# Optimization experiments

Measured on AMD Instinct MI355X. Metric: run time of the kernel, lower is better.

## Reference

```python
import jax, jax.numpy as jnp
import numpy as np

B, S = 64, 1024
DC, DR, H, DA = 64, 64, 128, 128
NC, NQ, MC = 256, 10000, 4


def setup_inputs() -> dict:
    key = jax.random.key(0)
    ks = jax.random.split(key, 16)
    question_seq = jax.random.randint(ks[0], (B, S), 0, NQ)
    correctness_seq = jax.random.randint(ks[1], (B, S), 0, 2)
    q2c_table = jax.random.randint(ks[2], (NQ, MC), 0, NC)
    q2c_mask = jax.random.randint(ks[3], (NQ, MC), 0, 2).at[:, 0].set(1)  # >=1 concept per question
    sd = 0.02
    concept_embed = jax.random.normal(ks[4], (NC, DC), jnp.float32) * sd
    correctness_embed = jax.random.normal(ks[5], (2, DR), jnp.float32) * sd
    mlp_w = jax.random.normal(ks[6], (DA, H), jnp.float32) * (1.0 / np.sqrt(H))
    mlp_b = jnp.zeros((DA,), jnp.float32)
    sim_w = jax.random.normal(ks[7], (1, DA), jnp.float32) * (1.0 / np.sqrt(DA))
    DIN = DC + DR
    W_ih = jax.random.normal(ks[8], (3 * H, DIN), jnp.float32) * (1.0 / np.sqrt(H))
    b_ih = jnp.zeros((3 * H,), jnp.float32)
    W_hh = jax.random.normal(ks[9], (3 * H, H), jnp.float32) * (1.0 / np.sqrt(H))
    b_hh = jnp.zeros((3 * H,), jnp.float32)
    pred_w = jax.random.normal(ks[10], (1, 2 * H + DC), jnp.float32) * (1.0 / np.sqrt(2 * H + DC))
    pred_b = jnp.zeros((1,), jnp.float32)
    return dict(question_seq=question_seq, correctness_seq=correctness_seq,
                q2c_table=q2c_table, q2c_mask=q2c_mask,
                concept_embed=concept_embed, correctness_embed=correctness_embed,
                mlp_w=mlp_w, mlp_b=mlp_b, sim_w=sim_w,
                W_ih=W_ih, b_ih=b_ih, W_hh=W_hh, b_hh=b_hh,
                pred_w=pred_w, pred_b=pred_b)


def _concept_emb(question_seq, q2c_table, q2c_mask, concept_embed):
    # fused question->concept embedding: masked mean over mapped concepts
    cids = q2c_table[question_seq]                      # [B,S,MC]
    m = q2c_mask[question_seq].astype(jnp.float32)      # [B,S,MC]
    ce = concept_embed[cids]                            # [B,S,MC,DC]
    return (ce * m[..., None]).sum(2) / jnp.clip(m.sum(2), 1.0)[..., None]


def _gru(x, W_ih, b_ih, W_hh, b_hh):
    # torch nn.GRU equations, batch_first; x: [B,S,DIN] -> [B,S,H]
    Xp = jnp.einsum('bsd,gd->bsg', x, W_ih) + b_ih      # [B,S,3H]
    h0 = jnp.zeros((x.shape[0], H), x.dtype)

    def step(h, gi):
        gh = h @ W_hh.T + b_hh
        i_r, i_z, i_n = jnp.split(gi, 3, axis=-1)
        h_r, h_z, h_n = jnp.split(gh, 3, axis=-1)
        r = jax.nn.sigmoid(i_r + h_r)
        z = jax.nn.sigmoid(i_z + h_z)
        n = jnp.tanh(i_n + r * h_n)
        h_new = (1.0 - z) * n + z * h
        return h_new, h_new

    _, hs = jax.lax.scan(step, h0, Xp.transpose(1, 0, 2))
    return hs.transpose(1, 0, 2)


def _attention(rnn_out, mlp_w, mlp_b, sim_w):
    # additive per-key score, causal softmax, bmm, exclusive cumsum, concat
    s = jnp.einsum('bsa,oa->bso', jnp.tanh(jnp.einsum('bsh,ah->bsa', rnn_out, mlp_w) + mlp_b), sim_w)[..., 0]  # [B,S]
    seq = rnn_out.shape[1]
    causal = jnp.tril(jnp.ones((seq, seq), bool))       # keep j<=i
    scores = jnp.where(causal[None], s[:, None, :], -jnp.inf)  # [B,S,S]
    alphas = jax.nn.softmax(scores, axis=-1)
    attn = jnp.einsum('bij,bjh->bih', alphas, rnn_out)  # [B,S,H]
    excl = jnp.cumsum(attn, axis=1) - attn              # exclusive cumsum
    return jnp.concatenate([excl, rnn_out], axis=-1)    # [B,S,2H]


def reference(question_seq, correctness_seq, q2c_table, q2c_mask,
              concept_embed, correctness_embed, mlp_w, mlp_b, sim_w,
              W_ih, b_ih, W_hh, b_hh, pred_w, pred_b):
    concept = _concept_emb(question_seq, q2c_table, q2c_mask, concept_embed)  # [B,S,DC]
    corr = correctness_embed[correctness_seq]                                  # [B,S,DR]
    cc = jnp.concatenate([concept, corr], -1)
    rc = jnp.concatenate([corr, concept], -1)
    inter = jnp.where((correctness_seq == 1)[..., None], cc, rc)               # [B,S,DC+DR]
    rnn_out = _gru(inter, W_ih, b_ih, W_hh, b_hh)                              # [B,S,H]
    latent = _attention(rnn_out, mlp_w, mlp_b, sim_w)                          # [B,S,2H]
    pin = jnp.concatenate([latent[:, :-1], concept[:, 1:]], axis=-1)           # [B,S-1,2H+DC]
    logits = jnp.einsum('bsd,od->bso', pin, pred_w) + pred_b
    return jax.nn.sigmoid(logits)[..., 0]                                      # [B,S-1]
```

## Files before the change

### kernel.cpp

```cpp
#include <hip/hip_runtime.h>
#include <hip/hip_bf16.h>
#include <cstdint>

#define BB 64
#define SS 1024
#define DCn 64
#define Hn 128
#define G3 384
#define HPITCH 144

using f32x4 = __attribute__((ext_vector_type(4))) float;
using bf16x8 = __attribute__((ext_vector_type(8))) short;

__device__ __forceinline__ float sigmoid_f(float x) {
  return __builtin_amdgcn_rcpf(1.0f + __expf(-x));
}
__device__ __forceinline__ float tanh_f(float x) {
  float xc = fminf(fmaxf(x, -15.0f), 15.0f);
  float t = __expf(-2.0f * xc);
  return (1.0f - t) * __builtin_amdgcn_rcpf(1.0f + t);
}
__device__ __forceinline__ short f2bf(float x) {
  union { float f; uint32_t u; } v; v.f = x;
  uint32_t r = v.u + 0x7FFFu + ((v.u >> 16) & 1u);
  return (short)(r >> 16);
}
__device__ __forceinline__ float bf2f(ushort u) {
  union { uint32_t i; float f; } v; v.i = (uint32_t)u << 16; return v.f;
}
__device__ __forceinline__ float sel4(f32x4 v, int q) {
  float t0 = (q & 1) ? v[1] : v[0];
  float t1 = (q & 1) ? v[3] : v[2];
  return (q & 2) ? t1 : t0;
}

#define LDS_BARRIER() do {                                   \
    asm volatile("s_waitcnt lgkmcnt(0)" ::: "memory");       \
    __builtin_amdgcn_s_barrier();                            \
    __builtin_amdgcn_sched_barrier(0);                       \
  } while (0)

__global__ __launch_bounds__(256) void convw_kernel(
    const float* __restrict__ W_ih, const float* __restrict__ mlp_w,
    const float* __restrict__ pred_w,
    ushort* __restrict__ Wihb, ushort* __restrict__ Baug) {
  int i = blockIdx.x * 256 + threadIdx.x;
  if (i < 49152) { Wihb[i] = (ushort)f2bf(W_ih[i]); return; }
  int j = i - 49152;
  int r = j >> 7, k = j & 127;
  float v = (r < 128) ? mlp_w[j]
          : (r == 128) ? pred_w[k]
          : (r == 129) ? pred_w[128 + k] : 0.0f;
  Baug[j] = (ushort)f2bf(v);
}

__global__ __launch_bounds__(256) void embed_kernel(
    const int* __restrict__ qseq, const int* __restrict__ cseq,
    const int* __restrict__ q2c, const int* __restrict__ q2cm,
    const float* __restrict__ cemb, const float* __restrict__ remb,
    const float* __restrict__ pred_w,
    ushort* __restrict__ interb, float* __restrict__ C3) {
  int pos = blockIdx.x * 2 + (threadIdx.x >> 7);
  int d = threadIdx.x & 127;
  int q = qseq[pos];
  int corr = cseq[pos];
  float val;
  if (d < 64) {
    float acc = 0.f, msum = 0.f;
#pragma unroll
    for (int c = 0; c < 4; ++c) {
      int id = q2c[q * 4 + c];
      float m = (float)q2cm[q * 4 + c];
      acc += m * cemb[id * 64 + d];
      msum += m;
    }
    val = acc / fmaxf(msum, 1.0f);
    float p3 = val * pred_w[256 + d];
#pragma unroll
    for (int o = 32; o; o >>= 1) p3 += __shfl_down(p3, o);
    if (d == 0) C3[pos] = p3;
  } else {
    val = remb[corr * 64 + (d - 64)];
  }
  int slot = (corr == 1) ? d : ((d < 64) ? d + 64 : d - 64);
  interb[(size_t)pos * 128 + slot] = (ushort)f2bf(val);
}

__global__ __launch_bounds__(256) void gemm_mfma_kernel(
    const ushort* __restrict__ Ap, const ushort* __restrict__ Bp,
    const float* __restrict__ bias, ushort* __restrict__ Cp, int N) {
  __shared__ bf16x8 Al[64][16];
  __shared__ bf16x8 Bl[64][16];
  const int m0 = blockIdx.x * 64, n0 = blockIdx.y * 64;
  const int tid = threadIdx.x;
  const int row = tid >> 2, j0 = (tid & 3) * 4;
  {
    const bf16x8* A = (const bf16x8*)Ap + (size_t)(m0 + row) * 16 + j0;
#pragma unroll
    for (int jj = 0; jj < 4; ++jj) Al[row][(j0 + jj) ^ (row & 15)] = A[jj];
    const bf16x8* Bg = (const bf16x8*)Bp + (size_t)(n0 + row) * 16 + j0;
#pragma unroll
    for (int jj = 0; jj < 4; ++jj) Bl[row][(j0 + jj) ^ (row & 15)] = Bg[jj];
  }
  __syncthreads();
  const int w = tid >> 6, lane = tid & 63, ln = lane & 15, cc = lane >> 4;
  bf16x8 bfr[4];
#pragma unroll
  for (int ks = 0; ks < 4; ++ks) bfr[ks] = Bl[w * 16 + ln][(ks * 4 + cc) ^ ln];
  f32x4 C0 = {0,0,0,0}, C1 = {0,0,0,0}, C2 = {0,0,0,0}, C3v = {0,0,0,0};
#pragma unroll
  for (int ks = 0; ks < 4; ++ks) {
    bf16x8 a0 = Al[0 * 16 + ln][(ks * 4 + cc) ^ ln];
    bf16x8 a1 = Al[1 * 16 + ln][(ks * 4 + cc) ^ ln];
    bf16x8 a2 = Al[2 * 16 + ln][(ks * 4 + cc) ^ ln];
    bf16x8 a3 = Al[3 * 16 + ln][(ks * 4 + cc) ^ ln];
    C0 = __builtin_amdgcn_mfma_f32_16x16x32_bf16(a0, bfr[ks], C0, 0, 0, 0);
    C1 = __builtin_amdgcn_mfma_f32_16x16x32_bf16(a1, bfr[ks], C1, 0, 0, 0);
    C2 = __builtin_amdgcn_mfma_f32_16x16x32_bf16(a2, bfr[ks], C2, 0, 0, 0);
    C3v = __builtin_amdgcn_mfma_f32_16x16x32_bf16(a3, bfr[ks], C3v, 0, 0, 0);
  }
  const float bv = bias[n0 + w * 16 + ln];
  const size_t ncol = n0 + w * 16 + ln;
#pragma unroll
  for (int rt = 0; rt < 4; ++rt) {
    f32x4 Cf = (rt == 0) ? C0 : (rt == 1) ? C1 : (rt == 2) ? C2 : C3v;
#pragma unroll
    for (int q = 0; q < 4; ++q)
      Cp[(size_t)(m0 + rt * 16 + cc * 4 + q) * N + ncol] = (ushort)f2bf(Cf[q] + bv);
  }
}

__global__ __attribute__((amdgpu_flat_work_group_size(512, 512)))
__attribute__((amdgpu_waves_per_eu(2, 2))) void gru_kernel(
    const ushort* __restrict__ Xp, const float* __restrict__ W_hh,
    const float* __restrict__ b_hh, float* __restrict__ rnn_out) {
  const int tid = threadIdx.x;
  const int w = tid >> 6;
  const int lane = tid & 63;
  const int ln = lane & 15;
  const int c = lane >> 4;
  const int bl = ln & 3;
  const int qs = ln >> 2;
  const int b0 = blockIdx.x * 4;

  __shared__ alignas(16) short hlds[2][4 * HPITCH];

  bf16x8 wf[3][4];
#pragma unroll
  for (int gt = 0; gt < 3; ++gt) {
    const float* wr = W_hh + (size_t)(gt * 128 + w * 16 + ln) * 128 + c * 8;
#pragma unroll
    for (int ks = 0; ks < 4; ++ks) {
      bf16x8 f;
#pragma unroll
      for (int j = 0; j < 8; ++j) f[j] = f2bf(wr[ks * 32 + j]);
      wf[gt][ks] = f;
    }
  }
  const f32x4 br = *(const f32x4*)(b_hh + w * 16 + c * 4);
  const f32x4 bz = *(const f32x4*)(b_hh + 128 + w * 16 + c * 4);
  const f32x4 bn = *(const f32x4*)(b_hh + 256 + w * 16 + c * 4);

  for (int i = tid; i < 576; i += 512) ((uint32_t*)hlds)[i] = 0;

  const int dim = w * 16 + c * 4 + qs;
  const ushort* xs = Xp + (size_t)(b0 + bl) * SS * G3 + dim;
  float* rsp = rnn_out + (size_t)(b0 + bl) * SS * Hn + dim;

  ushort xr0 = xs[0], xz0 = xs[128], xn0 = xs[256];
  ushort xr1 = xs[G3 + 0], xz1 = xs[G3 + 128], xn1 = xs[G3 + 256];
  const ushort* xpf = xs + 2 * (size_t)G3;

  float h_old = 0.0f;
  LDS_BARRIER();

#define GRU_STEP(RB, XR, XZ, XN)                                             \
  {                                                                          \
    const short* hr = hlds[RB] + bl * HPITCH;                                \
    bf16x8 h0 = *(const bf16x8*)(hr + 0 * 32 + c * 8);                       \
    bf16x8 h1 = *(const bf16x8*)(hr + 1 * 32 + c * 8);                       \
    bf16x8 h2 = *(const bf16x8*)(hr + 2 * 32 + c * 8);                       \
    bf16x8 h3 = *(const bf16x8*)(hr + 3 * 32 + c * 8);                       \
    ushort pr = xpf[0], pz = xpf[128], pn = xpf[256];                        \
    xpf += G3;                                                               \
    __builtin_amdgcn_s_setprio(1);                                           \
    f32x4 ar = br, az = bz, an = bn;                                         \
    ar = __builtin_amdgcn_mfma_f32_16x16x32_bf16(wf[0][0], h0, ar, 0, 0, 0); \
    an = __builtin_amdgcn_mfma_f32_16x16x32_bf16(wf[2][0], h0, an, 0, 0, 0); \
    ar = __builtin_amdgcn_mfma_f32_16x16x32_bf16(wf[0][1], h1, ar, 0, 0, 0); \
    an = __builtin_amdgcn_mfma_f32_16x16x32_bf16(wf[2][1], h1, an, 0, 0, 0); \
    ar = __builtin_amdgcn_mfma_f32_16x16x32_bf16(wf[0][2], h2, ar, 0, 0, 0); \
    an = __builtin_amdgcn_mfma_f32_16x16x32_bf16(wf[2][2], h2, an, 0, 0, 0); \
    ar = __builtin_amdgcn_mfma_f32_16x16x32_bf16(wf[0][3], h3, ar, 0, 0, 0); \
    an = __builtin_amdgcn_mfma_f32_16x16x32_bf16(wf[2][3], h3, an, 0, 0, 0); \
    az = __builtin_amdgcn_mfma_f32_16x16x32_bf16(wf[1][0], h0, az, 0, 0, 0); \
    az = __builtin_amdgcn_mfma_f32_16x16x32_bf16(wf[1][1], h1, az, 0, 0, 0); \
    az = __builtin_amdgcn_mfma_f32_16x16x32_bf16(wf[1][2], h2, az, 0, 0, 0); \
    az = __builtin_amdgcn_mfma_f32_16x16x32_bf16(wf[1][3], h3, az, 0, 0, 0); \
    __builtin_amdgcn_s_setprio(0);                                           \
    float ga = sel4(ar, qs), gz = sel4(az, qs), gn = sel4(an, qs);           \
    float r = sigmoid_f(bf2f(XR) + ga);                                      \
    float a = bf2f(XN) + r * gn;                                             \
    float e = __expf(-2.0f * a);                                             \
    float n = 2.0f * __builtin_amdgcn_rcpf(1.0f + e) - 1.0f;                 \
    float z = sigmoid_f(bf2f(XZ) + gz);                                      \
    float hn = n + z * (h_old - n);                                          \
    h_old = hn;                                                              \
    hlds[RB ^ 1][bl * HPITCH + dim] = f2bf(hn);                              \
    LDS_BARRIER();                                                           \
    *rsp = hn;                                                               \
    rsp += Hn;                                                               \
    XR = pr; XZ = pz; XN = pn;                                               \
  }

  for (int t = 0; t < SS; t += 2) {
    GRU_STEP(0, xr0, xz0, xn0)
    GRU_STEP(1, xr1, xz1, xn1)
  }
#undef GRU_STEP
}

__global__ __launch_bounds__(256) void gemm_score_kernel(
    const float* __restrict__ rnn, const ushort* __restrict__ Baug,
    const float* __restrict__ mlp_b, const float* __restrict__ sim_w,
    float* __restrict__ s, float* __restrict__ D1, float* __restrict__ D2) {
  __shared__ bf16x8 Al[64][16];
  __shared__ bf16x8 Bl[144][16];
  __shared__ float srow[64][4];
  const int m0 = blockIdx.x * 64;
  const int tid = threadIdx.x;
  {
    const int row = tid >> 2, j0 = (tid & 3) * 4;
    const float* A = rnn + (size_t)(m0 + row) * 128 + j0 * 8;
#pragma unroll
    for (int jj = 0; jj < 4; ++jj) {
      f32x4 lo = *(const f32x4*)(A + jj * 8);
      f32x4 hi = *(const f32x4*)(A + jj * 8 + 4);
      bf16x8 v;
#pragma unroll
      for (int q = 0; q < 4; ++q) { v[q] = f2bf(lo[q]); v[4 + q] = f2bf(hi[q]); }
      Al[row][(j0 + jj) ^ (row & 15)] = v;
    }
  }
  {
    const bf16x8* Bg = (const bf16x8*)Baug;
    for (int i = tid; i < 144 * 16; i += 256) {
      int r = i >> 4, j = i & 15;
      Bl[r][j ^ (r & 15)] = Bg[i];
    }
  }
  __syncthreads();
  const int w = tid >> 6, lane = tid & 63, ln = lane & 15, cc = lane >> 4;
  float racc[4][4] = {};
  for (int nt = w; nt < 9; nt += 4) {
    bf16x8 bfr[4];
#pragma unroll
    for (int ks = 0; ks < 4; ++ks) bfr[ks] = Bl[nt * 16 + ln][(ks * 4 + cc) ^ ln];
    f32x4 C0 = {0,0,0,0}, C1 = {0,0,0,0}, C2 = {0,0,0,0}, C3v = {0,0,0,0};
#pragma unroll
    for (int ks = 0; ks < 4; ++ks) {
      bf16x8 a0 = Al[0 * 16 + ln][(ks * 4 + cc) ^ ln];
      bf16x8 a1 = Al[1 * 16 + ln][(ks * 4 + cc) ^ ln];
      bf16x8 a2 = Al[2 * 16 + ln][(ks * 4 + cc) ^ ln];
      bf16x8 a3 = Al[3 * 16 + ln][(ks * 4 + cc) ^ ln];
      C0 = __builtin_amdgcn_mfma_f32_16x16x32_bf16(a0, bfr[ks], C0, 0, 0, 0);
      C1 = __builtin_amdgcn_mfma_f32_16x16x32_bf16(a1, bfr[ks], C1, 0, 0, 0);
      C2 = __builtin_amdgcn_mfma_f32_16x16x32_bf16(a2, bfr[ks], C2, 0, 0, 0);
      C3v = __builtin_amdgcn_mfma_f32_16x16x32_bf16(a3, bfr[ks], C3v, 0, 0, 0);
    }
    if (nt < 8) {
      const int col = nt * 16 + ln;
      const float bv = mlp_b[col];
      const float sw = sim_w[col];
#pragma unroll
      for (int rt = 0; rt < 4; ++rt) {
        f32x4 Cf = (rt == 0) ? C0 : (rt == 1) ? C1 : (rt == 2) ? C2 : C3v;
#pragma unroll
        for (int q = 0; q < 4; ++q)
          racc[rt][q] += tanh_f(Cf[q] + bv) * sw;
      }
    } else if (ln < 2) {
      float* Dp = (ln == 0) ? D1 : D2;
#pragma unroll
      for (int rt = 0; rt < 4; ++rt) {
        f32x4 Cf = (rt == 0) ? C0 : (rt == 1) ? C1 : (rt == 2) ? C2 : C3v;
#pragma unroll
        for (int q = 0; q < 4; ++q)
          Dp[m0 + rt * 16 + cc * 4 + q] = Cf[q];
      }
    }
  }
#pragma unroll
  for (int o = 1; o <= 8; o <<= 1)
#pragma unroll
    for (int rt = 0; rt < 4; ++rt)
#pragma unroll
      for (int q = 0; q < 4; ++q)
        racc[rt][q] += __shfl_xor(racc[rt][q], o);
  if (ln == 0)
#pragma unroll
    for (int rt = 0; rt < 4; ++rt)
#pragma unroll
      for (int q = 0; q < 4; ++q)
        srow[rt * 16 + cc * 4 + q][w] = racc[rt][q];
  __syncthreads();
  if (tid < 64)
    s[m0 + tid] = srow[tid][0] + srow[tid][1] + srow[tid][2] + srow[tid][3];
}

__global__ __launch_bounds__(128) void attn_final_kernel(
    const float* __restrict__ s, const float* __restrict__ D1,
    const float* __restrict__ D2, const float* __restrict__ C3,
    const float* __restrict__ pred_b, float* __restrict__ out) {
  const int b = blockIdx.x;
  const int tid = threadIdx.x;
  __shared__ float elds[SS];
  __shared__ float rcpd[SS];
  __shared__ float d1l[SS];
  __shared__ float dcl[SS];
  __shared__ float red[2];
  __shared__ float wtot[2];
  const float pb = pred_b[0];
  const float* sb = s + (size_t)b * SS;
  const float* d1b = D1 + (size_t)b * SS;
  const float* d2b = D2 + (size_t)b * SS;
  const float* c3b = C3 + (size_t)b * SS;
  float m = -1e30f;
  for (int i = tid; i < SS; i += 128) m = fmaxf(m, sb[i]);
#pragma unroll
  for (int o = 32; o; o >>= 1) m = fmaxf(m, __shfl_xor(m, o));
  if ((tid & 63) == 0) red[tid >> 6] = m;
  __syncthreads();
  m = fmaxf(red[0], red[1]);
  for (int i = tid; i < SS; i += 128) {
    elds[i] = __expf(sb[i] - m);
    d1l[i] = d1b[i];
    dcl[i] = d2b[i] + ((i < SS - 1) ? c3b[i + 1] : 0.0f) + pb;
  }
  __syncthreads();
  {
    const int base = tid * 8;
    float v[8];
    float run = 0.f;
#pragma unroll
    for (int k = 0; k < 8; ++k) { run += elds[base + k]; v[k] = run; }
    float tot = run, sc = tot;
#pragma unroll
    for (int o = 1; o < 64; o <<= 1) {
      float u = __shfl_up(sc, o);
      if ((tid & 63) >= o) sc += u;
    }
    if ((tid & 63) == 63) wtot[tid >> 6] = sc;
    __syncthreads();
    float excl = sc - tot;
    if (tid >= 64) excl += wtot[0];
#pragma unroll
    for (int k = 0; k < 8; ++k)
      rcpd[base + k] = __builtin_amdgcn_rcpf(v[k] + excl);
  }
  __syncthreads();
  float P_num = 0.f, P_run = 0.f;
  float* ob = out + (size_t)b * (SS - 1);
  for (int t = 0; t < SS; t += 4) {
    f32x4 e4 = *(const f32x4*)&elds[t];
    f32x4 r4 = *(const f32x4*)&rcpd[t];
    f32x4 d4 = *(const f32x4*)&d1l[t];
    f32x4 c4 = *(const f32x4*)&dcl[t];
#pragma unroll
    for (int k = 0; k < 4; ++k) {
      P_num += e4[k] * d4[k];
      float v = sigmoid_f(P_run + c4[k]);
      if (tid == 0 && (t + k) < SS - 1) ob[t + k] = v;
      P_run += P_num * r4[k];
    }
  }
}

extern "C" void kernel_launch(void* const* d_in, const int* in_sizes, int n_in,
                              void* d_out, int out_size, void* d_ws, size_t ws_size,
                              hipStream_t stream) {
  const int* qseq = (const int*)d_in[0];
  const int* cseq = (const int*)d_in[1];
  const int* q2c = (const int*)d_in[2];
  const int* q2cm = (const int*)d_in[3];
  const float* cemb = (const float*)d_in[4];
  const float* remb = (const float*)d_in[5];
  const float* mlp_w = (const float*)d_in[6];
  const float* mlp_b = (const float*)d_in[7];
  const float* sim_w = (const float*)d_in[8];
  const float* W_ih = (const float*)d_in[9];
  const float* b_ih = (const float*)d_in[10];
  const float* W_hh = (const float*)d_in[11];
  const float* b_hh = (const float*)d_in[12];
  const float* pred_w = (const float*)d_in[13];
  const float* pred_b = (const float*)d_in[14];
  float* out = (float*)d_out;

  float* ws = (float*)d_ws;
  ushort* interb = (ushort*)ws;
  ushort* Xp = (ushort*)(ws + 4194304);
  float* rnn = ws + 16777216;
  ushort* Wihb = (ushort*)(ws + 25165824);
  ushort* Baug = (ushort*)(ws + 25190400);
  float* sbuf = ws + 25199616;
  float* D1 = ws + 25265152;
  float* D2 = ws + 25330688;
  float* C3 = ws + 25396224;

  convw_kernel<<<264, 256, 0, stream>>>(W_ih, mlp_w, pred_w, Wihb, Baug);
  embed_kernel<<<32768, 256, 0, stream>>>(qseq, cseq, q2c, q2cm, cemb, remb,
                                          pred_w, interb, C3);
  gemm_mfma_kernel<<<dim3(1024, 6), 256, 0, stream>>>(interb, Wihb, b_ih, Xp, 384);
  gru_kernel<<<16, 512, 0, stream>>>(Xp, W_hh, b_hh, rnn);
  gemm_score_kernel<<<1024, 256, 0, stream>>>(rnn, Baug, mlp_b, sim_w,
                                              sbuf, D1, D2);
  attn_final_kernel<<<64, 128, 0, stream>>>(sbuf, D1, D2, C3, pred_b, out);
}
```

Baseline: 509.4 us.

## Fuse embedding into input-projection GEMM and store GRU output as bf16

Embedding gather and the W_ih projection GEMM now run in one kernel: each 512-thread block builds its 64-row bf16 input tile directly in LDS and multiplies it against the full 384-column W_ih held in LDS. This removes the interb round trip through global memory and one kernel launch. Separately, the GRU writes its hidden-state output as bf16 instead of fp32, so the score GEMM loads bf16 directly and skips its conversion step. The costs are a larger LDS footprint per block and a serialized embedding phase before the MFMA work.

```diff
diff --git a/kernel.cpp b/kernel.cpp
--- a/kernel.cpp
+++ b/kernel.cpp
@@ -54,86 +54,87 @@
   Baug[j] = (ushort)f2bf(v);
 }
 
-__global__ __launch_bounds__(256) void embed_kernel(
+__global__ __attribute__((amdgpu_flat_work_group_size(512, 512))) void embgemm_kernel(
     const int* __restrict__ qseq, const int* __restrict__ cseq,
     const int* __restrict__ q2c, const int* __restrict__ q2cm,
     const float* __restrict__ cemb, const float* __restrict__ remb,
-    const float* __restrict__ pred_w,
-    ushort* __restrict__ interb, float* __restrict__ C3) {
-  int pos = blockIdx.x * 2 + (threadIdx.x >> 7);
-  int d = threadIdx.x & 127;
-  int q = qseq[pos];
-  int corr = cseq[pos];
-  float val;
-  if (d < 64) {
-    float acc = 0.f, msum = 0.f;
-#pragma unroll
-    for (int c = 0; c < 4; ++c) {
-      int id = q2c[q * 4 + c];
-      float m = (float)q2cm[q * 4 + c];
-      acc += m * cemb[id * 64 + d];
-      msum += m;
-    }
-    val = acc / fmaxf(msum, 1.0f);
-    float p3 = val * pred_w[256 + d];
-#pragma unroll
-    for (int o = 32; o; o >>= 1) p3 += __shfl_down(p3, o);
-    if (d == 0) C3[pos] = p3;
-  } else {
-    val = remb[corr * 64 + (d - 64)];
-  }
-  int slot = (corr == 1) ? d : ((d < 64) ? d + 64 : d - 64);
-  interb[(size_t)pos * 128 + slot] = (ushort)f2bf(val);
-}
-
-__global__ __launch_bounds__(256) void gemm_mfma_kernel(
-    const ushort* __restrict__ Ap, const ushort* __restrict__ Bp,
-    const float* __restrict__ bias, ushort* __restrict__ Cp, int N) {
+    const float* __restrict__ pred_w, const ushort* __restrict__ Wihb,
+    const float* __restrict__ b_ih,
+    ushort* __restrict__ Xp, float* __restrict__ C3) {
   __shared__ bf16x8 Al[64][16];
-  __shared__ bf16x8 Bl[64][16];
-  const int m0 = blockIdx.x * 64, n0 = blockIdx.y * 64;
+  __shared__ bf16x8 Bl[384][16];
+  const int m0 = blockIdx.x * 64;
   const int tid = threadIdx.x;
-  const int row = tid >> 2, j0 = (tid & 3) * 4;
   {
-    const bf16x8* A = (const bf16x8*)Ap + (size_t)(m0 + row) * 16 + j0;
-#pragma unroll
-    for (int jj = 0; jj < 4; ++jj) Al[row][(j0 + jj) ^ (row & 15)] = A[jj];
-    const bf16x8* Bg = (const bf16x8*)Bp + (size_t)(n0 + row) * 16 + j0;
-#pragma unroll
-    for (int jj = 0; jj < 4; ++jj) Bl[row][(j0 + jj) ^ (row & 15)] = Bg[jj];
+    const bf16x8* Bg = (const bf16x8*)Wihb;
+    for (int i = tid; i < 384 * 16; i += 512) {
+      int r = i >> 4, j = i & 15;
+      Bl[r][j ^ (r & 15)] = Bg[i];
+    }
+  }
+  ushort* Alus = (ushort*)Al;
+  for (int it = 0; it < 16; ++it) {
+    int prow = it * 4 + (tid >> 7);
+    int pos = m0 + prow;
+    int d = tid & 127;
+    int q = qseq[pos];
+    int corr = cseq[pos];
+    float val;
+    if (d < 64) {
+      float acc = 0.f, msum = 0.f;
+#pragma unroll
+      for (int c = 0; c < 4; ++c) {
+        int id = q2c[q * 4 + c];
+        float m = (float)q2cm[q * 4 + c];
+        acc += m * cemb[id * 64 + d];
+        msum += m;
+      }
+      val = acc / fmaxf(msum, 1.0f);
+      float p3 = val * pred_w[256 + d];
+#pragma unroll
+      for (int o = 32; o; o >>= 1) p3 += __shfl_down(p3, o);
+      if (d == 0) C3[pos] = p3;
+    } else {
+      val = remb[corr * 64 + (d - 64)];
+    }
+    int slot = (corr == 1) ? d : ((d < 64) ? d + 64 : d - 64);
+    Alus[prow * 128 + (((slot >> 3) ^ (prow & 15)) << 3) + (slot & 7)] =
+        (ushort)f2bf(val);
   }
   __syncthreads();
   const int w = tid >> 6, lane = tid & 63, ln = lane & 15, cc = lane >> 4;
-  bf16x8 bfr[4];
-#pragma unroll
-  for (int ks = 0; ks < 4; ++ks) bfr[ks] = Bl[w * 16 + ln][(ks * 4 + cc) ^ ln];
-  f32x4 C0 = {0,0,0,0}, C1 = {0,0,0,0}, C2 = {0,0,0,0}, C3v = {0,0,0,0};
-#pragma unroll
-  for (int ks = 0; ks < 4; ++ks) {
-    bf16x8 a0 = Al[0 * 16 + ln][(ks * 4 + cc) ^ ln];
-    bf16x8 a1 = Al[1 * 16 + ln][(ks * 4 + cc) ^ ln];
-    bf16x8 a2 = Al[2 * 16 + ln][(ks * 4 + cc) ^ ln];
-    bf16x8 a3 = Al[3 * 16 + ln][(ks * 4 + cc) ^ ln];
-    C0 = __builtin_amdgcn_mfma_f32_16x16x32_bf16(a0, bfr[ks], C0, 0, 0, 0);
-    C1 = __builtin_amdgcn_mfma_f32_16x16x32_bf16(a1, bfr[ks], C1, 0, 0, 0);
-    C2 = __builtin_amdgcn_mfma_f32_16x16x32_bf16(a2, bfr[ks], C2, 0, 0, 0);
-    C3v = __builtin_amdgcn_mfma_f32_16x16x32_bf16(a3, bfr[ks], C3v, 0, 0, 0);
-  }
-  const float bv = bias[n0 + w * 16 + ln];
-  const size_t ncol = n0 + w * 16 + ln;
-#pragma unroll
-  for (int rt = 0; rt < 4; ++rt) {
-    f32x4 Cf = (rt == 0) ? C0 : (rt == 1) ? C1 : (rt == 2) ? C2 : C3v;
-#pragma unroll
-    for (int q = 0; q < 4; ++q)
-      Cp[(size_t)(m0 + rt * 16 + cc * 4 + q) * N + ncol] = (ushort)f2bf(Cf[q] + bv);
+  for (int nt = w; nt < 24; nt += 8) {
+    bf16x8 bfr[4];
+#pragma unroll
+    for (int ks = 0; ks < 4; ++ks) bfr[ks] = Bl[nt * 16 + ln][(ks * 4 + cc) ^ ln];
+    f32x4 C0 = {0,0,0,0}, C1 = {0,0,0,0}, C2 = {0,0,0,0}, C3v = {0,0,0,0};
+#pragma unroll
+    for (int ks = 0; ks < 4; ++ks) {
+      bf16x8 a0 = Al[0 * 16 + ln][(ks * 4 + cc) ^ ln];
+      bf16x8 a1 = Al[1 * 16 + ln][(ks * 4 + cc) ^ ln];
+      bf16x8 a2 = Al[2 * 16 + ln][(ks * 4 + cc) ^ ln];
+      bf16x8 a3 = Al[3 * 16 + ln][(ks * 4 + cc) ^ ln];
+      C0 = __builtin_amdgcn_mfma_f32_16x16x32_bf16(a0, bfr[ks], C0, 0, 0, 0);
+      C1 = __builtin_amdgcn_mfma_f32_16x16x32_bf16(a1, bfr[ks], C1, 0, 0, 0);
+      C2 = __builtin_amdgcn_mfma_f32_16x16x32_bf16(a2, bfr[ks], C2, 0, 0, 0);
+      C3v = __builtin_amdgcn_mfma_f32_16x16x32_bf16(a3, bfr[ks], C3v, 0, 0, 0);
+    }
+    const int col = nt * 16 + ln;
+    const float bv = b_ih[col];
+#pragma unroll
+    for (int rt = 0; rt < 4; ++rt) {
+      f32x4 Cf = (rt == 0) ? C0 : (rt == 1) ? C1 : (rt == 2) ? C2 : C3v;
+#pragma unroll
+      for (int q = 0; q < 4; ++q)
+        Xp[(size_t)(m0 + rt * 16 + cc * 4 + q) * G3 + col] = (ushort)f2bf(Cf[q] + bv);
+    }
   }
 }
 
 __global__ __attribute__((amdgpu_flat_work_group_size(512, 512)))
 __attribute__((amdgpu_waves_per_eu(2, 2))) void gru_kernel(
     const ushort* __restrict__ Xp, const float* __restrict__ W_hh,
-    const float* __restrict__ b_hh, float* __restrict__ rnn_out) {
+    const float* __restrict__ b_hh, ushort* __restrict__ rnn_out) {
   const int tid = threadIdx.x;
   const int w = tid >> 6;
   const int lane = tid & 63;
@@ -165,7 +166,7 @@
 
   const int dim = w * 16 + c * 4 + qs;
   const ushort* xs = Xp + (size_t)(b0 + bl) * SS * G3 + dim;
-  float* rsp = rnn_out + (size_t)(b0 + bl) * SS * Hn + dim;
+  ushort* rsp = rnn_out + (size_t)(b0 + bl) * SS * Hn + dim;
 
   ushort xr0 = xs[0], xz0 = xs[128], xn0 = xs[256];
   ushort xr1 = xs[G3 + 0], xz1 = xs[G3 + 128], xn1 = xs[G3 + 256];
@@ -206,9 +207,10 @@
     float z = sigmoid_f(bf2f(XZ) + gz);                                      \
     float hn = n + z * (h_old - n);                                          \
     h_old = hn;                                                              \
-    hlds[RB ^ 1][bl * HPITCH + dim] = f2bf(hn);                              \
+    ushort hb = (ushort)f2bf(hn);                                            \
+    hlds[RB ^ 1][bl * HPITCH + dim] = (short)hb;                             \
     LDS_BARRIER();                                                           \
-    *rsp = hn;                                                               \
+    *rsp = hb;                                                               \
     rsp += Hn;                                                               \
     XR = pr; XZ = pz; XN = pn;                                               \
   }
@@ -221,7 +223,7 @@
 }
 
 __global__ __launch_bounds__(256) void gemm_score_kernel(
-    const float* __restrict__ rnn, const ushort* __restrict__ Baug,
+    const ushort* __restrict__ rnn, const ushort* __restrict__ Baug,
     const float* __restrict__ mlp_b, const float* __restrict__ sim_w,
     float* __restrict__ s, float* __restrict__ D1, float* __restrict__ D2) {
   __shared__ bf16x8 Al[64][16];
@@ -231,16 +233,9 @@
   const int tid = threadIdx.x;
   {
     const int row = tid >> 2, j0 = (tid & 3) * 4;
-    const float* A = rnn + (size_t)(m0 + row) * 128 + j0 * 8;
-#pragma unroll
-    for (int jj = 0; jj < 4; ++jj) {
-      f32x4 lo = *(const f32x4*)(A + jj * 8);
-      f32x4 hi = *(const f32x4*)(A + jj * 8 + 4);
-      bf16x8 v;
-#pragma unroll
-      for (int q = 0; q < 4; ++q) { v[q] = f2bf(lo[q]); v[4 + q] = f2bf(hi[q]); }
-      Al[row][(j0 + jj) ^ (row & 15)] = v;
-    }
+    const bf16x8* A = (const bf16x8*)rnn + (size_t)(m0 + row) * 16 + j0;
+#pragma unroll
+    for (int jj = 0; jj < 4; ++jj) Al[row][(j0 + jj) ^ (row & 15)] = A[jj];
   }
   {
     const bf16x8* Bg = (const bf16x8*)Baug;
@@ -397,9 +392,8 @@
   float* out = (float*)d_out;
 
   float* ws = (float*)d_ws;
-  ushort* interb = (ushort*)ws;
   ushort* Xp = (ushort*)(ws + 4194304);
-  float* rnn = ws + 16777216;
+  ushort* rnn = (ushort*)(ws + 16777216);
   ushort* Wihb = (ushort*)(ws + 25165824);
   ushort* Baug = (ushort*)(ws + 25190400);
   float* sbuf = ws + 25199616;
@@ -408,9 +402,8 @@
   float* C3 = ws + 25396224;
 
   convw_kernel<<<264, 256, 0, stream>>>(W_ih, mlp_w, pred_w, Wihb, Baug);
-  embed_kernel<<<32768, 256, 0, stream>>>(qseq, cseq, q2c, q2cm, cemb, remb,
-                                          pred_w, interb, C3);
-  gemm_mfma_kernel<<<dim3(1024, 6), 256, 0, stream>>>(interb, Wihb, b_ih, Xp, 384);
+  embgemm_kernel<<<1024, 512, 0, stream>>>(qseq, cseq, q2c, q2cm, cemb, remb,
+                                           pred_w, Wihb, b_ih, Xp, C3);
   gru_kernel<<<16, 512, 0, stream>>>(Xp, W_hh, b_hh, rnn);
   gemm_score_kernel<<<1024, 256, 0, stream>>>(rnn, Baug, mlp_b, sim_w,
                                               sbuf, D1, D2);
```

After: 548.4 us. +7.7%, slower.
